# Kernel optimization log

Hardware: AMD Instinct MI355X
Metric: run time of the kernel (lower is better)

The kernel has to match this reference:

```python
import jax, jax.numpy as jnp
import numpy as np

N, D, H = 4_000_000, 10, 16

def setup_inputs() -> dict:
    key = jax.random.key(0)
    k1, k2, k3, k4, k5 = jax.random.split(key, 5)
    x = jax.random.normal(k1, (N, D), dtype=jnp.float32)
    # torch nn.Linear default init: U(-1/sqrt(fan_in), 1/sqrt(fan_in))
    lim1 = 1.0 / np.sqrt(D)
    lim2 = 1.0 / np.sqrt(H)
    W1 = jax.random.uniform(k2, (H, D), dtype=jnp.float32, minval=-lim1, maxval=lim1)
    b1 = jax.random.uniform(k3, (H,), dtype=jnp.float32, minval=-lim1, maxval=lim1)
    W2 = jax.random.uniform(k4, (1, H), dtype=jnp.float32, minval=-lim2, maxval=lim2)
    b2 = jax.random.uniform(k5, (1,), dtype=jnp.float32, minval=-lim2, maxval=lim2)
    return {"x": x, "W1": W1, "b1": b1, "W2": W2, "b2": b2}

def reference(x, W1, b1, W2, b2):
    gram = x.T @ x                      # [10,10] symmetric Gram matrix
    v, w = jnp.linalg.eigh(gram)        # eigenvalues ascending; w: [10,10]
    y = jnp.maximum(w @ W1.T + b1, 0.0) # fc1 + ReLU -> [10,16]
    y = y @ W2.T + b2                   # fc2 -> [10,1]
    return 0.5 * (jax.nn.sigmoid(y) + 1.0)
```

## Files before the change

### kernel.cpp

```cpp
#include <hip/hip_runtime.h>
#include <math.h>


#define BLK2 256
#define GRID2 1024
#define TILE_F4 (BLK2 * 5)

__global__ void zero_ws_kernel(double* __restrict__ g) {
  int t = threadIdx.x;
  if (t < 220) g[t] = 0.0;
}

__global__ __launch_bounds__(BLK2) void gram_kernel(const float4* __restrict__ x4,
                                                    double* __restrict__ g,
                                                    int nf4) {
  __shared__ float4 tile[TILE_F4];
  float acc[55];
#pragma unroll
  for (int k = 0; k < 55; k++) acc[k] = 0.0f;

  const int tid = threadIdx.x;
  const int ntiles = (nf4 + TILE_F4 - 1) / TILE_F4;

  for (int t = blockIdx.x; t < ntiles; t += GRID2) {
    const int base = t * TILE_F4;
    float4 r0, r1, r2, r3, r4;
    {
      int i0 = base + 0 * BLK2 + tid;
      int i1 = base + 1 * BLK2 + tid;
      int i2 = base + 2 * BLK2 + tid;
      int i3 = base + 3 * BLK2 + tid;
      int i4 = base + 4 * BLK2 + tid;
      float4 zz = make_float4(0.f, 0.f, 0.f, 0.f);
      r0 = (i0 < nf4) ? x4[i0] : zz;
      r1 = (i1 < nf4) ? x4[i1] : zz;
      r2 = (i2 < nf4) ? x4[i2] : zz;
      r3 = (i3 < nf4) ? x4[i3] : zz;
      r4 = (i4 < nf4) ? x4[i4] : zz;
    }
    __syncthreads();
    tile[0 * BLK2 + tid] = r0;
    tile[1 * BLK2 + tid] = r1;
    tile[2 * BLK2 + tid] = r2;
    tile[3 * BLK2 + tid] = r3;
    tile[4 * BLK2 + tid] = r4;
    __syncthreads();
    float4 q0 = tile[tid * 5 + 0];
    float4 q1 = tile[tid * 5 + 1];
    float4 q2 = tile[tid * 5 + 2];
    float4 q3 = tile[tid * 5 + 3];
    float4 q4 = tile[tid * 5 + 4];
    float v[20] = {q0.x, q0.y, q0.z, q0.w, q1.x, q1.y, q1.z, q1.w,
                   q2.x, q2.y, q2.z, q2.w, q3.x, q3.y, q3.z, q3.w,
                   q4.x, q4.y, q4.z, q4.w};
    int k = 0;
#pragma unroll
    for (int i = 0; i < 10; i++) {
#pragma unroll
      for (int j = 0; j <= i; j++) {
        acc[k] += v[i] * v[j] + v[10 + i] * v[10 + j];
        k++;
      }
    }
  }

  __shared__ double sred[4][55];
  int lane = threadIdx.x & 63;
  int wv = threadIdx.x >> 6;
#pragma unroll
  for (int k = 0; k < 55; k++) {
    double d = (double)acc[k];
#pragma unroll
    for (int off = 32; off > 0; off >>= 1) d += __shfl_down(d, off, 64);
    if (lane == 0) sred[wv][k] = d;
  }
  __syncthreads();
  double* gr = g + 55 * (blockIdx.x & 3);
  if (threadIdx.x < 55) {
    double s = sred[0][threadIdx.x] + sred[1][threadIdx.x] +
               sred[2][threadIdx.x] + sred[3][threadIdx.x];
    atomicAdd(&gr[threadIdx.x], s);
  }
}


__device__ __forceinline__ float sf_sign(float a, float b) {
  return (b >= 0.0f) ? fabsf(a) : -fabsf(a);
}

__device__ __forceinline__ float slapy2(float x, float y) {
  float xa = fabsf(x), ya = fabsf(y);
  float w = fmaxf(xa, ya), z = fminf(xa, ya);
  if (z == 0.0f) return w;
  float q = z / w;
  return w * sqrtf(1.0f + q * q);
}

__device__ __forceinline__ void slartg(float f, float g, float* c, float* s, float* r) {
  if (g == 0.0f) {
    *c = 1.0f; *s = 0.0f; *r = f;
  } else if (f == 0.0f) {
    *c = 0.0f; *s = sf_sign(1.0f, g); *r = fabsf(g);
  } else {
    float d = sqrtf(f * f + g * g);
    *c = fabsf(f) / d;
    float rr = sf_sign(d, f);
    *s = g / rr;
    *r = rr;
  }
}

__device__ __forceinline__ void slaev2(float a, float b, float c,
                                       float* rt1, float* rt2, float* cs1, float* sn1) {
  float sm = a + c;
  float df = a - c;
  float adf = fabsf(df);
  float tb = b + b;
  float ab = fabsf(tb);
  float acmx, acmn;
  if (fabsf(a) > fabsf(c)) { acmx = a; acmn = c; } else { acmx = c; acmn = a; }
  float rt;
  if (adf > ab)      { float t = ab / adf; rt = adf * sqrtf(1.0f + t * t); }
  else if (adf < ab) { float t = adf / ab; rt = ab * sqrtf(1.0f + t * t); }
  else               { rt = ab * sqrtf(2.0f); }
  int sgn1;
  if (sm < 0.0f) {
    *rt1 = 0.5f * (sm - rt); sgn1 = -1;
    *rt2 = (acmx / *rt1) * acmn - (b / *rt1) * b;
  } else if (sm > 0.0f) {
    *rt1 = 0.5f * (sm + rt); sgn1 = 1;
    *rt2 = (acmx / *rt1) * acmn - (b / *rt1) * b;
  } else {
    *rt1 = 0.5f * rt; *rt2 = -0.5f * rt; sgn1 = 1;
  }
  int sgn2;
  float cs;
  if (df >= 0.0f) { cs = df + rt; sgn2 = 1; } else { cs = df - rt; sgn2 = -1; }
  float acs = fabsf(cs);
  if (acs > ab) {
    float ct = -tb / cs;
    *sn1 = 1.0f / sqrtf(1.0f + ct * ct);
    *cs1 = ct * (*sn1);
  } else {
    if (ab == 0.0f) { *cs1 = 1.0f; *sn1 = 0.0f; }
    else {
      float tn = -cs / tb;
      *cs1 = 1.0f / sqrtf(1.0f + tn * tn);
      *sn1 = tn * (*cs1);
    }
  }
  if (sgn1 == sgn2) { float tn = *cs1; *cs1 = -(*sn1); *sn1 = tn; }
}

__device__ __forceinline__ float sel10(const float* a, int idx0) {
  float v = 0.0f;
#pragma unroll
  for (int k = 0; k < 10; k++) v = (k == idx0) ? a[k] : v;
  return v;
}
__device__ __forceinline__ void put10(float* a, int idx0, float v) {
#pragma unroll
  for (int k = 0; k < 10; k++) a[k] = (k == idx0) ? v : a[k];
}

#define A_(r, c) Am[((r)-1) * 10 + ((c)-1)]
#define Z_(r, c) Zm[((r)-1) * 10 + ((c)-1)]
#define D_(i) dv[(i)-1]
#define E_(i) ev[(i)-1]
#define TAUV(i) tauv[(i)-1]
#define WV(i) wvv[(i)-1]

__global__ __launch_bounds__(64, 1) void eig_mlp_kernel(
    const double* __restrict__ g,
    const float* __restrict__ W1,
    const float* __restrict__ b1,
    const float* __restrict__ W2,
    const float* __restrict__ b2,
    float* __restrict__ out) {
  if (blockIdx.x != 0) return;
  const int lane = threadIdx.x;
  const int n = 10;
  float Am[100], Zm[100];
  float dv[10], ev[10], tauv[10], wvv[10], csv[10], snv[10];

  {
    int k = 0;
#pragma unroll
    for (int i = 0; i < 10; i++)
#pragma unroll
      for (int j = 0; j <= i; j++) {
        double v = g[k] + g[55 + k] + g[110 + k] + g[165 + k];
        float f = (float)v;
        Am[i * 10 + j] = f;
        Am[j * 10 + i] = f;
        k++;
      }
  }

#pragma unroll
  for (int i = 1; i <= n - 1; i++) {
    const int nmi = n - i;
    float alpha = A_(i + 1, i);
    float taui = 0.0f;
    if (nmi > 1) {
      float ss = 0.0f;
#pragma unroll
      for (int r = i + 2; r <= n; r++) { float t = A_(r, i); ss += t * t; }
      float xnorm = sqrtf(ss);
      if (xnorm != 0.0f) {
        float beta = -sf_sign(slapy2(alpha, xnorm), alpha);
        taui = (beta - alpha) / beta;
        float sc = 1.0f / (alpha - beta);
#pragma unroll
        for (int r = i + 2; r <= n; r++) A_(r, i) *= sc;
        alpha = beta;
      }
    }
    E_(i) = alpha;
    A_(i + 1, i) = alpha;
    if (taui != 0.0f) {
      A_(i + 1, i) = 1.0f;
#pragma unroll
      for (int r = i + 1; r <= n; r++) {
        float s = 0.0f;
#pragma unroll
        for (int c = i + 1; c <= n; c++) {
          float arc = (r >= c) ? A_(r, c) : A_(c, r);
          s += arc * A_(c, i);
        }
        WV(r) = taui * s;
      }
      float dot = 0.0f;
#pragma unroll
      for (int r = i + 1; r <= n; r++) dot += WV(r) * A_(r, i);
      float al2 = -0.5f * taui * dot;
#pragma unroll
      for (int r = i + 1; r <= n; r++) WV(r) += al2 * A_(r, i);
#pragma unroll
      for (int c = i + 1; c <= n; c++)
#pragma unroll
        for (int r = c; r <= n; r++)
          A_(r, c) -= A_(r, i) * WV(c) + WV(r) * A_(c, i);
      A_(i + 1, i) = E_(i);
    }
    D_(i) = A_(i, i);
    TAUV(i) = taui;
  }
  D_(n) = A_(n, n);

#pragma unroll
  for (int r = 1; r <= n; r++)
#pragma unroll
    for (int c = 1; c <= n; c++) Z_(r, c) = (r == c) ? 1.0f : 0.0f;
#pragma unroll
  for (int i = n - 1; i >= 1; i--) {
    float taui = TAUV(i);
    if (taui != 0.0f) {
#pragma unroll
      for (int c = 1; c <= n; c++) {
        float t = Z_(i + 1, c);
#pragma unroll
        for (int r = i + 2; r <= n; r++) t += A_(r, i) * Z_(r, c);
        t *= taui;
        Z_(i + 1, c) -= t;
#pragma unroll
        for (int r = i + 2; r <= n; r++) Z_(r, c) -= A_(r, i) * t;
      }
    }
  }

  const int r_own = (lane < 10) ? lane : 0;
  float z[10];
#pragma unroll
  for (int k = 0; k < 10; k++) {
    float v = Zm[0 * 10 + k];
#pragma unroll
    for (int rr = 1; rr < 10; rr++) v = (r_own == rr) ? Zm[rr * 10 + k] : v;
    z[k] = v;
  }

  const float eps = 5.9604644775390625e-08f;
  const float eps2 = eps * eps;
  const float safmin = 1.17549435082228751e-38f;
  const int nmaxit = n * 30;
  int jtot = 0;
  int l1 = 1;
  int guard = 0;

  while (l1 <= n && guard++ < 2000) {
    if (l1 > 1) put10(ev, l1 - 2, 0.0f);
    int m = n;
    {
      bool found = false;
#pragma unroll
      for (int k = 1; k <= n - 1; k++) {
        if (!found && k >= l1) {
          float tst = fabsf(ev[k - 1]);
          if (tst == 0.0f) {
            m = k; found = true;
          } else if (tst <= (sqrtf(fabsf(dv[k - 1])) * sqrtf(fabsf(dv[k]))) * eps) {
            ev[k - 1] = 0.0f;
            m = k; found = true;
          }
        }
      }
    }
    int l = l1, lsv = l, lend = m, lendsv = m;
    l1 = m + 1;
    if (lend == l) continue;
    if (fabsf(sel10(dv, lend - 1)) < fabsf(sel10(dv, l - 1))) { lend = lsv; l = lendsv; }

    if (lend > l) {
      for (;;) {
        if (guard++ > 4000) break;
        int m2 = lend;
        if (l != lend) {
          bool fnd = false;
#pragma unroll
          for (int k = 1; k <= n - 1; k++) {
            if (!fnd && k >= l && k <= lend - 1) {
              float e = ev[k - 1];
              if (e * e <= (eps2 * fabsf(dv[k - 1])) * fabsf(dv[k]) + safmin) {
                m2 = k; fnd = true;
              }
            }
          }
        }
        if (m2 < lend) put10(ev, m2 - 1, 0.0f);
        float p = sel10(dv, l - 1);
        if (m2 == l) {
          put10(dv, l - 1, p);
          l = l + 1;
          if (l <= lend) continue;
          break;
        }
        if (m2 == l + 1) {
          float rt1, rt2, c2, s2;
          slaev2(sel10(dv, l - 1), sel10(ev, l - 1), sel10(dv, l), &rt1, &rt2, &c2, &s2);
          float a = sel10(z, l);
          float b = sel10(z, l - 1);
          put10(z, l, c2 * a - s2 * b);
          put10(z, l - 1, s2 * a + c2 * b);
          put10(dv, l - 1, rt1);
          put10(dv, l, rt2);
          put10(ev, l - 1, 0.0f);
          l = l + 2;
          if (l <= lend) continue;
          break;
        }
        if (jtot == nmaxit) break;
        jtot++;
        float El = sel10(ev, l - 1);
        float gg = (sel10(dv, l) - p) / (2.0f * El);
        float rr = slapy2(gg, 1.0f);
        gg = sel10(dv, m2 - 1) - p + (El / (gg + sf_sign(rr, gg)));
        float s = 1.0f, c = 1.0f;
        p = 0.0f;
#pragma unroll
        for (int i = n - 1; i >= 1; i--) {
          if (i <= m2 - 1 && i >= l) {
            float e = ev[i - 1];
            float f = s * e, b = c * e;
            slartg(gg, f, &c, &s, &rr);
            if (i != m2 - 1) ev[i] = rr;
            gg = dv[i] - p;
            rr = (dv[i - 1] - gg) * s + 2.0f * c * b;
            p = s * rr;
            dv[i] = gg + p;
            gg = c * rr - b;
            csv[i - 1] = c;
            snv[i - 1] = -s;
          }
        }
        {
          float a = sel10(z, m2 - 1);
#pragma unroll
          for (int j = n - 1; j >= 1; j--) {
            if (j <= m2 - 1 && j >= l) {
              float cj = csv[j - 1], sj = snv[j - 1];
              float b = z[j - 1];
              z[j] = cj * a - sj * b;
              a = sj * a + cj * b;
            }
          }
          put10(z, l - 1, a);
        }
        put10(dv, l - 1, sel10(dv, l - 1) - p);
        put10(ev, l - 1, gg);
      }
    } else {
      for (;;) {
        if (guard++ > 4000) break;
        int m2 = lend;
        if (l != lend) {
          bool fnd = false;
#pragma unroll
          for (int k = n; k >= 2; k--) {
            if (!fnd && k <= l && k >= lend + 1) {
              float e = ev[k - 2];
              if (e * e <= (eps2 * fabsf(dv[k - 1])) * fabsf(dv[k - 2]) + safmin) {
                m2 = k; fnd = true;
              }
            }
          }
        }
        if (m2 > lend) put10(ev, m2 - 2, 0.0f);
        float p = sel10(dv, l - 1);
        if (m2 == l) {
          put10(dv, l - 1, p);
          l = l - 1;
          if (l >= lend) continue;
          break;
        }
        if (m2 == l - 1) {
          float rt1, rt2, c2, s2;
          slaev2(sel10(dv, l - 2), sel10(ev, l - 2), sel10(dv, l - 1), &rt1, &rt2, &c2, &s2);
          float a = sel10(z, l - 1);
          float b = sel10(z, l - 2);
          put10(z, l - 1, c2 * a - s2 * b);
          put10(z, l - 2, s2 * a + c2 * b);
          put10(dv, l - 2, rt1);
          put10(dv, l - 1, rt2);
          put10(ev, l - 2, 0.0f);
          l = l - 2;
          if (l >= lend) continue;
          break;
        }
        if (jtot == nmaxit) break;
        jtot++;
        float El1 = sel10(ev, l - 2);
        float gg = (sel10(dv, l - 2) - p) / (2.0f * El1);
        float rr = slapy2(gg, 1.0f);
        gg = sel10(dv, m2 - 1) - p + (El1 / (gg + sf_sign(rr, gg)));
        float s = 1.0f, c = 1.0f;
        p = 0.0f;
#pragma unroll
        for (int i = 1; i <= n - 1; i++) {
          if (i >= m2 && i <= l - 1) {
            float e = ev[i - 1];
            float f = s * e, b = c * e;
            slartg(gg, f, &c, &s, &rr);
            if (i >= 2) {
              if (i != m2) ev[i - 2] = rr;
            }
            gg = dv[i - 1] - p;
            rr = (dv[i] - gg) * s + 2.0f * c * b;
            p = s * rr;
            dv[i - 1] = gg + p;
            gg = c * rr - b;
            csv[i - 1] = c;
            snv[i - 1] = s;
          }
        }
        {
          float carry = sel10(z, m2 - 1);
#pragma unroll
          for (int j = 1; j <= n - 1; j++) {
            if (j >= m2 && j <= l - 1) {
              float cj = csv[j - 1], sj = snv[j - 1];
              float t = z[j];
              z[j - 1] = sj * t + cj * carry;
              carry = cj * t - sj * carry;
            }
          }
          put10(z, l - 1, carry);
        }
        put10(dv, l - 1, sel10(dv, l - 1) - p);
        put10(ev, l - 2, gg);
      }
    }
  }

  for (int ii = 2; ii <= n; ii++) {
    int i = ii - 1;
    int k = i;
    float p = sel10(dv, i - 1);
    for (int j = ii; j <= n; j++) {
      float dj = sel10(dv, j - 1);
      if (dj < p) { k = j; p = dj; }
    }
    if (k != i) {
      float di = sel10(dv, i - 1);
      put10(dv, k - 1, di);
      put10(dv, i - 1, p);
      float a = sel10(z, i - 1), b = sel10(z, k - 1);
      put10(z, i - 1, b);
      put10(z, k - 1, a);
    }
  }

  if (lane < 10) {
    double o = (double)b2[0];
#pragma unroll
    for (int h = 0; h < 16; h++) {
      double sgm = (double)b1[h];
#pragma unroll
      for (int k = 0; k < 10; k++) sgm += (double)z[k] * (double)W1[h * 10 + k];
      if (sgm > 0.0) o += sgm * (double)W2[h];
    }
    double sig = 1.0 / (1.0 + exp(-o));
    out[lane] = (float)(0.5 * (sig + 1.0));
  }
}

extern "C" void kernel_launch(void* const* d_in, const int* in_sizes, int n_in,
                              void* d_out, int out_size, void* d_ws, size_t ws_size,
                              hipStream_t stream) {
  const float* x  = (const float*)d_in[0];
  const float* W1 = (const float*)d_in[1];
  const float* b1 = (const float*)d_in[2];
  const float* W2 = (const float*)d_in[3];
  const float* b2 = (const float*)d_in[4];
  double* g = (double*)d_ws;
  float* out = (float*)d_out;

  int nf4 = in_sizes[0] / 4;

  zero_ws_kernel<<<1, 256, 0, stream>>>(g);
  gram_kernel<<<GRID2, BLK2, 0, stream>>>((const float4*)x, g, nf4);
  eig_mlp_kernel<<<1, 64, 0, stream>>>(g, W1, b1, W2, b2, out);
}
```

Baseline: 338.5 us.

## Load gram rows directly per thread with register double-buffered prefetch

The gram kernel no longer stages tiles through shared memory with two barriers per iteration. Each thread now loads its own five contiguous float4s (two rows) straight from global memory, and the next tile is prefetched into registers while the current one is accumulated. This removes LDS traffic and syncs and overlaps loads with FMAs. The cost is strided, less coalesced global access (stride of 80 bytes per lane) and higher register pressure.

```diff
diff --git a/kernel.cpp b/kernel.cpp
--- a/kernel.cpp
+++ b/kernel.cpp
@@ -14,45 +14,43 @@
 __global__ __launch_bounds__(BLK2) void gram_kernel(const float4* __restrict__ x4,
                                                     double* __restrict__ g,
                                                     int nf4) {
-  __shared__ float4 tile[TILE_F4];
   float acc[55];
 #pragma unroll
   for (int k = 0; k < 55; k++) acc[k] = 0.0f;
 
   const int tid = threadIdx.x;
   const int ntiles = (nf4 + TILE_F4 - 1) / TILE_F4;
-
-  for (int t = blockIdx.x; t < ntiles; t += GRID2) {
-    const int base = t * TILE_F4;
-    float4 r0, r1, r2, r3, r4;
-    {
-      int i0 = base + 0 * BLK2 + tid;
-      int i1 = base + 1 * BLK2 + tid;
-      int i2 = base + 2 * BLK2 + tid;
-      int i3 = base + 3 * BLK2 + tid;
-      int i4 = base + 4 * BLK2 + tid;
-      float4 zz = make_float4(0.f, 0.f, 0.f, 0.f);
-      r0 = (i0 < nf4) ? x4[i0] : zz;
-      r1 = (i1 < nf4) ? x4[i1] : zz;
-      r2 = (i2 < nf4) ? x4[i2] : zz;
-      r3 = (i3 < nf4) ? x4[i3] : zz;
-      r4 = (i4 < nf4) ? x4[i4] : zz;
-    }
-    __syncthreads();
-    tile[0 * BLK2 + tid] = r0;
-    tile[1 * BLK2 + tid] = r1;
-    tile[2 * BLK2 + tid] = r2;
-    tile[3 * BLK2 + tid] = r3;
-    tile[4 * BLK2 + tid] = r4;
-    __syncthreads();
-    float4 q0 = tile[tid * 5 + 0];
-    float4 q1 = tile[tid * 5 + 1];
-    float4 q2 = tile[tid * 5 + 2];
-    float4 q3 = tile[tid * 5 + 3];
-    float4 q4 = tile[tid * 5 + 4];
-    float v[20] = {q0.x, q0.y, q0.z, q0.w, q1.x, q1.y, q1.z, q1.w,
-                   q2.x, q2.y, q2.z, q2.w, q3.x, q3.y, q3.z, q3.w,
-                   q4.x, q4.y, q4.z, q4.w};
+  const float4 zz = make_float4(0.f, 0.f, 0.f, 0.f);
+
+  int t = (int)blockIdx.x;
+  bool active = (t < ntiles);
+
+  float4 c0 = zz, c1 = zz, c2 = zz, c3 = zz, c4 = zz;
+  if (active) {
+    int b = t * TILE_F4 + tid * 5;
+    c0 = (b + 0 < nf4) ? x4[b + 0] : zz;
+    c1 = (b + 1 < nf4) ? x4[b + 1] : zz;
+    c2 = (b + 2 < nf4) ? x4[b + 2] : zz;
+    c3 = (b + 3 < nf4) ? x4[b + 3] : zz;
+    c4 = (b + 4 < nf4) ? x4[b + 4] : zz;
+  }
+
+  while (active) {
+    int tn = t + GRID2;
+    bool an = (tn < ntiles);
+    float4 n0 = zz, n1 = zz, n2 = zz, n3 = zz, n4 = zz;
+    if (an) {
+      int b = tn * TILE_F4 + tid * 5;
+      n0 = (b + 0 < nf4) ? x4[b + 0] : zz;
+      n1 = (b + 1 < nf4) ? x4[b + 1] : zz;
+      n2 = (b + 2 < nf4) ? x4[b + 2] : zz;
+      n3 = (b + 3 < nf4) ? x4[b + 3] : zz;
+      n4 = (b + 4 < nf4) ? x4[b + 4] : zz;
+    }
+
+    float v[20] = {c0.x, c0.y, c0.z, c0.w, c1.x, c1.y, c1.z, c1.w,
+                   c2.x, c2.y, c2.z, c2.w, c3.x, c3.y, c3.z, c3.w,
+                   c4.x, c4.y, c4.z, c4.w};
     int k = 0;
 #pragma unroll
     for (int i = 0; i < 10; i++) {
@@ -62,6 +60,10 @@
         k++;
       }
     }
+
+    c0 = n0; c1 = n1; c2 = n2; c3 = n3; c4 = n4;
+    t = tn;
+    active = an;
   }
 
   __shared__ double sred[4][55];
```

New measurement: 333.1 us. About the same (-1.6%).
